# Kernel tuning notes

Measured on AMD Instinct MI355X. Metric: run time of the kernel, lower is better.

Reference implementation:

```python
import jax, jax.numpy as jnp
import numpy as np

B, S, H, M, E = 8, 2048, 2048, 256, 8
Hh = H // 2

def setup_inputs() -> dict:
    key = jax.random.key(0)
    ks = jax.random.split(key, 12)
    s = 0.02
    return {
        "x":   jax.random.normal(ks[0], (B, S, H), dtype=jnp.float32),
        # metacognitive (router) network: H -> M -> M -> E, softmax
        "Wm1": jax.random.normal(ks[1], (H, M), dtype=jnp.float32) * s,
        "bm1": jnp.zeros((M,), dtype=jnp.float32),
        "Wm2": jax.random.normal(ks[2], (M, M), dtype=jnp.float32) * s,
        "bm2": jnp.zeros((M,), dtype=jnp.float32),
        "Wm3": jax.random.normal(ks[3], (M, E), dtype=jnp.float32) * s,
        "bm3": jnp.zeros((E,), dtype=jnp.float32),
        # stacked expert MLPs: Linear(H,H/2)-ReLU-Linear(H/2,H)-Tanh
        "W1":  jax.random.normal(ks[4], (E, H, Hh), dtype=jnp.float32) * s,
        "b1":  jnp.zeros((E, Hh), dtype=jnp.float32),
        "W2":  jax.random.normal(ks[5], (E, Hh, H), dtype=jnp.float32) * s,
        "b2":  jnp.zeros((E, H), dtype=jnp.float32),
        # strategy_effectiveness buffer (init: ones)
        "eff": jnp.ones((E,), dtype=jnp.float32),
    }

def reference(x, Wm1, bm1, Wm2, bm2, Wm3, bm3, W1, b1, W2, b2, eff):
    # --- select_strategy ---
    pooled = x.mean(axis=1)                                   # [B,H]
    h = jax.nn.relu(pooled @ Wm1 + bm1)                       # [B,M]
    h = jax.nn.relu(h @ Wm2 + bm2)                            # [B,M]
    probs = jax.nn.softmax(h @ Wm3 + bm3, axis=-1)            # [B,E]
    w = jax.nn.softmax(probs * eff[None, :], axis=-1)         # [B,E]
    # --- apply_strategies (all experts batched) ---
    he = jax.nn.relu(jnp.einsum('bsh,ehf->bsef', x, W1) + b1) # [B,S,E,Hh]
    ye = jnp.tanh(jnp.einsum('bsef,efh->bseh', he, W2) + b2)  # [B,S,E,H]
    out = jnp.einsum('bseh,be->bsh', ye, w)                   # [B,S,H]
    return out
```

## Files before the change

### kernel.cpp

```cpp
#include <hip/hip_runtime.h>
#include <hip/hip_bf16.h>
#include <cstdint>
#include <cstddef>

#define B_   8
#define S_   2048
#define H_   2048
#define M_   256
#define E_   8
#define HH_  1024
#define BS_  (B_*S_)

typedef _Float16 f16;
typedef _Float16 f16x8 __attribute__((ext_vector_type(8)));
typedef float    f32x4 __attribute__((ext_vector_type(4)));

#define SLOT_B   49152
#define A_HALF_B 16384
#define B_OFF    32768
#define B_HALF_B 8192

__device__ __forceinline__ void gl_lds16(const void* g, void* l) {
  __builtin_amdgcn_global_load_lds(
      (const __attribute__((address_space(1))) uint32_t*)g,
      (__attribute__((address_space(3))) uint32_t*)l, 16, 0, 0);
}

__device__ __forceinline__ int sinv(int P) {
  int b8 = (P >> 8) & 1, b7 = (P >> 7) & 1, b6 = (P >> 6) & 1;
  return P ^ (b8 << 6) ^ (b7 << 5) ^ ((b6 ^ b8) << 4);
}

__device__ __forceinline__ float fast_tanh(float x) {
  x = fminf(fmaxf(x, -15.f), 15.f);
  float t = __expf(2.f * x);
  return (t - 1.f) / (t + 1.f);
}

template<int NG, int NT_LG, int ASEG_SH, int BSEG_SH, class F>
__device__ __forceinline__ void kloop(const char* aS0, const char* aS1,
    const char* bS0, char* ldsc, int aRd, int bRd, int wv, int ln,
    f32x4 (&acc)[4][4], F fold) {
  constexpr int NT = 1 << NT_LG;

  auto stage = [&](int gs, int ss, int h) {
    int tt = gs & (NT - 1);
    size_t ea = 0, eb = 0;
    if constexpr (ASEG_SH != 0) {
      int e = gs >> NT_LG;
      ea = (size_t)e << ASEG_SH;
      eb = (size_t)e << BSEG_SH;
    }
    int koff = tt * 128 + h * 64;
    char* dA = ldsc + ss * SLOT_B + h * A_HALF_B + wv * 1024 + ln * 16;
    gl_lds16(aS0 + ea + koff, dA);
    gl_lds16(aS1 + ea + koff, dA + 8192);
    char* dB = ldsc + ss * SLOT_B + B_OFF + h * B_HALF_B + wv * 1024 + ln * 16;
    gl_lds16(bS0 + eb + koff, dB);
  };

#pragma unroll
  for (int t = 0; t < 2; ++t) { stage(t, t, 0); stage(t, t, 1); }
  asm volatile("s_waitcnt vmcnt(6)" ::: "memory");
  __builtin_amdgcn_s_barrier();

  int s = 0;
#pragma unroll 1
  for (int g = 0; g < NG; ++g) {
    int ss = s + 2; if (ss >= 3) ss -= 3;
    const char* sbase = ldsc + s * SLOT_B;
    __builtin_amdgcn_sched_barrier(0);

    f16x8 af[2][4], bf[2][4];
#pragma unroll
    for (int h = 0; h < 2; ++h) {
      const char* aB = sbase + h * A_HALF_B + aRd;
      const char* bB = sbase + B_OFF + h * B_HALF_B + bRd;
#pragma unroll
      for (int m = 0; m < 4; ++m) af[h][m] = *(const f16x8*)(aB + m * 1024);
#pragma unroll
      for (int n = 0; n < 4; ++n) bf[h][n] = *(const f16x8*)(bB + n * 1024);
    }

    if ((g + 2) < NG) { stage(g + 2, ss, 0); stage(g + 2, ss, 1); }

    __builtin_amdgcn_s_setprio(1);
#pragma unroll
    for (int h = 0; h < 2; ++h)
#pragma unroll
      for (int m = 0; m < 4; ++m)
#pragma unroll
        for (int n = 0; n < 4; ++n)
          acc[m][n] = __builtin_amdgcn_mfma_f32_16x16x32_f16(af[h][m], bf[h][n], acc[m][n], 0, 0, 0);
    __builtin_amdgcn_s_setprio(0);

    if ((g & (NT - 1)) == (NT - 1)) fold(g >> NT_LG);

    __builtin_amdgcn_sched_barrier(0);
    if (g < NG - 2) { asm volatile("s_waitcnt vmcnt(6)" ::: "memory"); }
    else            { asm volatile("s_waitcnt vmcnt(0)" ::: "memory"); }
    __builtin_amdgcn_s_barrier();
    ++s; if (s >= 3) s -= 3;
  }
}

__global__ __launch_bounds__(512, 2) void gemm1_pipe(
    const f16* __restrict__ xf, const f16* __restrict__ W1t,
    const float* __restrict__ b1, f16* __restrict__ he) {
  __shared__ f16 lds[3 * 24576];
  char* ldsc = (char*)lds;
  int tid = threadIdx.x, wv = tid >> 6, ln = tid & 63, l15 = ln & 15, kq = ln >> 4;
  int wr = wv >> 1, wc = wv & 1;

  int id = blockIdx.x;
  int logical = (id & 7) * 512 + (id >> 3);
  int nt = logical & 7, mt = (logical >> 3) & 63, e = logical >> 9;
  int brow = mt * 256, bcol = nt * 128;

  int mask = (ln & 7) << 4;
  int aRd = ((wr * 64 + l15) * 64 + kq * 16) ^ mask;
  int bRd = ((wc * 64 + l15) * 64 + kq * 16) ^ mask;

  int PA0 = wv * 1024 + ln * 16;
  int LA0 = sinv(PA0), LA1 = sinv(PA0 + 8192), LB = sinv(PA0);
  const char* aS0 = (const char*)xf + (size_t)(brow + (LA0 >> 6)) * (H_ * 2) + (LA0 & 63);
  const char* aS1 = (const char*)xf + (size_t)(brow + (LA1 >> 6)) * (H_ * 2) + (LA1 & 63);
  const char* bS0 = (const char*)W1t + ((size_t)e * HH_ + bcol + (LB >> 6)) * (H_ * 2) + (LB & 63);

  f32x4 acc[4][4] = {};
  kloop<32, 5, 0, 0>(aS0, aS1, bS0, ldsc, aRd, bRd, wv, ln, acc, [](int) {});

  f16* C = he + (size_t)e * BS_ * HH_;
#pragma unroll
  for (int n = 0; n < 4; ++n) {
    int gc = bcol + wc * 64 + n * 16 + l15;
    float bias = b1[e * HH_ + gc];
#pragma unroll
    for (int m = 0; m < 4; ++m) {
      int gr0 = brow + wr * 64 + m * 16 + kq * 4;
#pragma unroll
      for (int r = 0; r < 4; ++r)
        C[(size_t)(gr0 + r) * HH_ + gc] = (f16)fmaxf(acc[m][n][r] + bias, 0.f);
    }
  }
}

__global__ __launch_bounds__(512, 2) void gemm2_pipe(
    const f16* __restrict__ he, const f16* __restrict__ W2t,
    const float* __restrict__ b2, const float* __restrict__ wbuf,
    float* __restrict__ out) {
  __shared__ f16 lds[3 * 24576];
  __shared__ float biasLDS[E_][128];
  __shared__ float wLDS[E_];
  char* ldsc = (char*)lds;
  int tid = threadIdx.x, wv = tid >> 6, ln = tid & 63, l15 = ln & 15, kq = ln >> 4;
  int wr = wv >> 1, wc = wv & 1;

  int id = blockIdx.x;
  int logical = (id & 7) * 128 + (id >> 3);
  int nt = logical & 15, mt = logical >> 4;
  int brow = mt * 256, bcol = nt * 128;
  int bb = brow >> 11;

  {
    int i = tid;
#pragma unroll
    for (int rep = 0; rep < 2; ++rep, i += 512) {
      int e = i >> 7, c = i & 127;
      biasLDS[e][c] = b2[e * H_ + bcol + c];
    }
    if (tid < E_) wLDS[tid] = wbuf[bb * E_ + tid];
  }
  __syncthreads();

  int mask = (ln & 7) << 4;
  int aRd = ((wr * 64 + l15) * 64 + kq * 16) ^ mask;
  int bRd = ((wc * 64 + l15) * 64 + kq * 16) ^ mask;

  int PA0 = wv * 1024 + ln * 16;
  int LA0 = sinv(PA0), LA1 = sinv(PA0 + 8192), LB = sinv(PA0);
  const char* aS0 = (const char*)he + (size_t)(brow + (LA0 >> 6)) * (HH_ * 2) + (LA0 & 63);
  const char* aS1 = (const char*)he + (size_t)(brow + (LA1 >> 6)) * (HH_ * 2) + (LA1 & 63);
  const char* bS0 = (const char*)W2t + (size_t)(bcol + (LB >> 6)) * (HH_ * 2) + (LB & 63);

  f32x4 acc[4][4] = {};
  f32x4 tot[4][4] = {};

  auto fold = [&](int e) {
    float we = wLDS[e];
#pragma unroll
    for (int n = 0; n < 4; ++n) {
      float bias = biasLDS[e][wc * 64 + n * 16 + l15];
#pragma unroll
      for (int m = 0; m < 4; ++m) {
#pragma unroll
        for (int r = 0; r < 4; ++r) {
          tot[m][n][r] += we * fast_tanh(acc[m][n][r] + bias);
          acc[m][n][r] = 0.f;
        }
      }
    }
  };

  kloop<128, 4, 25, 22>(aS0, aS1, bS0, ldsc, aRd, bRd, wv, ln, acc, fold);

#pragma unroll
  for (int n = 0; n < 4; ++n) {
    int gc = bcol + wc * 64 + n * 16 + l15;
#pragma unroll
    for (int m = 0; m < 4; ++m) {
      int gr0 = brow + wr * 64 + m * 16 + kq * 4;
#pragma unroll
      for (int r = 0; r < 4; ++r)
        out[(size_t)(gr0 + r) * H_ + gc] = tot[m][n][r];
    }
  }
}

__global__ void convert_x_pool(const float* __restrict__ x, f16* __restrict__ xf,
                               float* __restrict__ partial) {
  int h  = blockIdx.x * 256 + threadIdx.x;
  int sc = blockIdx.y;
  int b  = blockIdx.z;
  size_t base = ((size_t)b * S_ + sc * 64) * H_ + h;
  float sum = 0.f;
#pragma unroll 4
  for (int i = 0; i < 64; ++i) {
    float v = x[base + (size_t)i * H_];
    sum += v;
    xf[base + (size_t)i * H_] = (f16)v;
  }
  partial[((size_t)b * H_ + h) * 32 + sc] = sum;
}

__global__ void pool_finalize(const float* __restrict__ partial, float* __restrict__ pooled) {
  int i = blockIdx.x * 256 + threadIdx.x;
  float s = 0.f;
#pragma unroll
  for (int c = 0; c < 32; ++c) s += partial[(size_t)i * 32 + c];
  pooled[i] = s * (1.0f / S_);
}

__global__ void router_kernel(const float* __restrict__ pooled,
                              const float* __restrict__ Wm1, const float* __restrict__ bm1,
                              const float* __restrict__ Wm2, const float* __restrict__ bm2,
                              const float* __restrict__ Wm3, const float* __restrict__ bm3,
                              const float* __restrict__ eff, float* __restrict__ wout) {
  __shared__ float pl[H_];
  __shared__ float h1[M_];
  __shared__ float h2[M_];
  __shared__ float lg[E_];
  int b = blockIdx.x;
  int t = threadIdx.x;

  for (int i = t; i < H_; i += 256) pl[i] = pooled[b * H_ + i];
  __syncthreads();

  float s = bm1[t];
  for (int k = 0; k < H_; ++k) s += pl[k] * Wm1[(size_t)k * M_ + t];
  h1[t] = fmaxf(s, 0.f);
  __syncthreads();

  s = bm2[t];
  for (int k = 0; k < M_; ++k) s += h1[k] * Wm2[k * M_ + t];
  h2[t] = fmaxf(s, 0.f);
  __syncthreads();

  if (t < E_) {
    float l = bm3[t];
    for (int k = 0; k < M_; ++k) l += h2[k] * Wm3[k * E_ + t];
    lg[t] = l;
  }
  __syncthreads();

  if (t == 0) {
    float p[E_], q[E_];
    float mx = -1e30f;
    for (int e = 0; e < E_; ++e) mx = fmaxf(mx, lg[e]);
    float den = 0.f;
    for (int e = 0; e < E_; ++e) { p[e] = __expf(lg[e] - mx); den += p[e]; }
    float inv = 1.f / den;
    for (int e = 0; e < E_; ++e) q[e] = p[e] * inv * eff[e];
    mx = -1e30f;
    for (int e = 0; e < E_; ++e) mx = fmaxf(mx, q[e]);
    den = 0.f;
    for (int e = 0; e < E_; ++e) { q[e] = __expf(q[e] - mx); den += q[e]; }
    inv = 1.f / den;
    for (int e = 0; e < E_; ++e) wout[b * E_ + e] = q[e] * inv;
  }
}

__global__ void transpose_cvt(const float* __restrict__ in, f16* __restrict__ out,
                              int R, int C) {
  __shared__ f16 tile[32][33];
  int e  = blockIdx.z;
  int c0 = blockIdx.x * 32, r0 = blockIdx.y * 32;
  int tx = threadIdx.x & 31, ty = threadIdx.x >> 5;
  const float* inp = in + (size_t)e * R * C;
  f16* outp = out + (size_t)e * R * C;
#pragma unroll
  for (int i = 0; i < 4; ++i) {
    int r = r0 + ty + i * 8;
    tile[ty + i * 8][tx] = (f16)inp[(size_t)r * C + c0 + tx];
  }
  __syncthreads();
#pragma unroll
  for (int i = 0; i < 4; ++i) {
    int c = c0 + ty + i * 8;
    outp[(size_t)c * R + r0 + tx] = tile[tx][ty + i * 8];
  }
}

extern "C" void kernel_launch(void* const* d_in, const int* in_sizes, int n_in,
                              void* d_out, int out_size, void* d_ws, size_t ws_size,
                              hipStream_t stream) {
  const float* x   = (const float*)d_in[0];
  const float* Wm1 = (const float*)d_in[1];
  const float* bm1 = (const float*)d_in[2];
  const float* Wm2 = (const float*)d_in[3];
  const float* bm2 = (const float*)d_in[4];
  const float* Wm3 = (const float*)d_in[5];
  const float* bm3 = (const float*)d_in[6];
  const float* W1  = (const float*)d_in[7];
  const float* b1  = (const float*)d_in[8];
  const float* W2  = (const float*)d_in[9];
  const float* b2  = (const float*)d_in[10];
  const float* eff = (const float*)d_in[11];
  float* out = (float*)d_out;

  char* ws = (char*)d_ws;
  size_t off = 0;
  auto take = [&](size_t bytes) { void* p = ws + off; off += (bytes + 255) & ~(size_t)255; return p; };

  f16*   xf      = (f16*)  take((size_t)BS_ * H_ * 2);
  f16*   W1t     = (f16*)  take((size_t)E_ * HH_ * H_ * 2);
  f16*   W2t     = (f16*)  take((size_t)E_ * H_ * HH_ * 2);
  float* partial = (float*)take((size_t)B_ * H_ * 32 * 4);
  float* pooled  = (float*)take((size_t)B_ * H_ * 4);
  float* wbuf    = (float*)take(1024);
  f16*   he      = (f16*)  take((size_t)E_ * BS_ * HH_ * 2);

  convert_x_pool<<<dim3(H_ / 256, S_ / 64, B_), 256, 0, stream>>>(x, xf, partial);
  pool_finalize<<<(B_ * H_) / 256, 256, 0, stream>>>(partial, pooled);
  router_kernel<<<B_, 256, 0, stream>>>(pooled, Wm1, bm1, Wm2, bm2, Wm3, bm3, eff, wbuf);
  transpose_cvt<<<dim3(HH_ / 32, H_ / 32, E_), 256, 0, stream>>>(W1, W1t, H_, HH_);
  transpose_cvt<<<dim3(H_ / 32, HH_ / 32, E_), 256, 0, stream>>>(W2, W2t, HH_, H_);

  gemm1_pipe<<<4096, 512, 0, stream>>>(xf, W1t, b1, he);
  gemm2_pipe<<<1024, 512, 0, stream>>>(he, W2t, b2, wbuf, out);
}
```

Measured before the change: 1.483 ms.

## Enlarge GEMM tiles to 256x256 with 4-slot half-K pipeline

Both expert GEMMs move from 256x128 to 256x256 block tiles, so each wave computes 128x64 (8x4 MFMA tiles) and operands are reused more per LDS load. The K-loop is restructured into 32-element half-steps across a 4-slot LDS ring with 3-ahead prefetch, a simpler XOR swizzle, and staging interleaved per M-half with extra barriers. The gemm2 running weighted-tanh accumulator is stored in fp16 to save registers, which lowers output precision. The larger accumulator footprint raises register pressure at two blocks per CU.

```diff
diff --git a/kernel.cpp b/kernel.cpp
--- a/kernel.cpp
+++ b/kernel.cpp
@@ -13,12 +13,10 @@
 
 typedef _Float16 f16;
 typedef _Float16 f16x8 __attribute__((ext_vector_type(8)));
+typedef _Float16 f16x4 __attribute__((ext_vector_type(4)));
 typedef float    f32x4 __attribute__((ext_vector_type(4)));
 
-#define SLOT_B   49152
-#define A_HALF_B 16384
-#define B_OFF    32768
-#define B_HALF_B 8192
+#define HSLOT 32768
 
 __device__ __forceinline__ void gl_lds16(const void* g, void* l) {
   __builtin_amdgcn_global_load_lds(
@@ -26,118 +24,126 @@
       (__attribute__((address_space(3))) uint32_t*)l, 16, 0, 0);
 }
 
-__device__ __forceinline__ int sinv(int P) {
-  int b8 = (P >> 8) & 1, b7 = (P >> 7) & 1, b6 = (P >> 6) & 1;
-  return P ^ (b8 << 6) ^ (b7 << 5) ^ ((b6 ^ b8) << 4);
-}
-
 __device__ __forceinline__ float fast_tanh(float x) {
   x = fminf(fmaxf(x, -15.f), 15.f);
   float t = __expf(2.f * x);
   return (t - 1.f) / (t + 1.f);
 }
 
-template<int NG, int NT_LG, int ASEG_SH, int BSEG_SH, class F>
-__device__ __forceinline__ void kloop(const char* aS0, const char* aS1,
-    const char* bS0, char* ldsc, int aRd, int bRd, int wv, int ln,
-    f32x4 (&acc)[4][4], F fold) {
-  constexpr int NT = 1 << NT_LG;
-
-  auto stage = [&](int gs, int ss, int h) {
-    int tt = gs & (NT - 1);
-    size_t ea = 0, eb = 0;
-    if constexpr (ASEG_SH != 0) {
-      int e = gs >> NT_LG;
-      ea = (size_t)e << ASEG_SH;
-      eb = (size_t)e << BSEG_SH;
-    }
-    int koff = tt * 128 + h * 64;
-    char* dA = ldsc + ss * SLOT_B + h * A_HALF_B + wv * 1024 + ln * 16;
-    gl_lds16(aS0 + ea + koff, dA);
-    gl_lds16(aS1 + ea + koff, dA + 8192);
-    char* dB = ldsc + ss * SLOT_B + B_OFF + h * B_HALF_B + wv * 1024 + ln * 16;
-    gl_lds16(bS0 + eb + koff, dB);
+template<int NG, bool SEG, int KB, class F>
+__device__ __forceinline__ void kloop(const char* aBlk, const char* bBlk,
+                                      char* ldsc, f32x4 (&acc)[8][4], F&& fold) {
+  constexpr int NH = NG * 2;
+  const int tid = threadIdx.x, ln = tid & 63, wv = tid >> 6;
+  const int l15 = ln & 15, kq = ln >> 4;
+  const int wm = wv >> 2, wn = wv & 3;
+
+  const char* aPc[2]; const char* bPc[2];
+#pragma unroll
+  for (int j = 0; j < 2; ++j) {
+    int row = (tid >> 2) + j * 128;
+    int kqs = (tid & 3) ^ ((row >> 1) & 3);
+    aPc[j] = aBlk + (size_t)row * KB + kqs * 16;
+    bPc[j] = bBlk + (size_t)row * KB + kqs * 16;
+  }
+  const int rowA = wm * 128 + l15;
+  const int rowB = wn * 64 + l15;
+  const int aRd = rowA * 64 + ((kq ^ ((rowA >> 1) & 3)) << 4);
+  const int bRd = 16384 + rowB * 64 + ((kq ^ ((rowB >> 1) & 3)) << 4);
+  const int dst0 = tid * 16;
+
+  auto stage2 = [&](int Ht, int op) {
+    if (Ht >= NH) return;
+    char* sb = ldsc + (Ht & 3) * HSLOT;
+    size_t oa, ob;
+    if constexpr (SEG) {
+      size_t kb = (size_t)((Ht & 31) * 64);
+      oa = ((size_t)(Ht >> 5) << 25) + kb;
+      ob = ((size_t)(Ht >> 5) << 22) + kb;
+    } else { oa = ob = (size_t)Ht * 64; }
+    if (op == 0) {
+      gl_lds16(aPc[0] + oa, sb + dst0);
+      gl_lds16(aPc[1] + oa, sb + 8192 + dst0);
+    } else {
+      gl_lds16(bPc[0] + ob, sb + 16384 + dst0);
+      gl_lds16(bPc[1] + ob, sb + 24576 + dst0);
+    }
   };
 
 #pragma unroll
-  for (int t = 0; t < 2; ++t) { stage(t, t, 0); stage(t, t, 1); }
-  asm volatile("s_waitcnt vmcnt(6)" ::: "memory");
+  for (int Ht = 0; Ht < 3; ++Ht) { stage2(Ht, 0); stage2(Ht, 1); }
+  asm volatile("s_waitcnt vmcnt(8)" ::: "memory");
   __builtin_amdgcn_s_barrier();
 
-  int s = 0;
 #pragma unroll 1
   for (int g = 0; g < NG; ++g) {
-    int ss = s + 2; if (ss >= 3) ss -= 3;
-    const char* sbase = ldsc + s * SLOT_B;
-    __builtin_amdgcn_sched_barrier(0);
-
-    f16x8 af[2][4], bf[2][4];
-#pragma unroll
-    for (int h = 0; h < 2; ++h) {
-      const char* aB = sbase + h * A_HALF_B + aRd;
-      const char* bB = sbase + B_OFF + h * B_HALF_B + bRd;
-#pragma unroll
-      for (int m = 0; m < 4; ++m) af[h][m] = *(const f16x8*)(aB + m * 1024);
-#pragma unroll
-      for (int n = 0; n < 4; ++n) bf[h][n] = *(const f16x8*)(bB + n * 1024);
-    }
-
-    if ((g + 2) < NG) { stage(g + 2, ss, 0); stage(g + 2, ss, 1); }
-
-    __builtin_amdgcn_s_setprio(1);
-#pragma unroll
-    for (int h = 0; h < 2; ++h)
-#pragma unroll
-      for (int m = 0; m < 4; ++m)
-#pragma unroll
-        for (int n = 0; n < 4; ++n)
-          acc[m][n] = __builtin_amdgcn_mfma_f32_16x16x32_f16(af[h][m], bf[h][n], acc[m][n], 0, 0, 0);
-    __builtin_amdgcn_s_setprio(0);
-
-    if ((g & (NT - 1)) == (NT - 1)) fold(g >> NT_LG);
-
-    __builtin_amdgcn_sched_barrier(0);
-    if (g < NG - 2) { asm volatile("s_waitcnt vmcnt(6)" ::: "memory"); }
-    else            { asm volatile("s_waitcnt vmcnt(0)" ::: "memory"); }
-    __builtin_amdgcn_s_barrier();
-    ++s; if (s >= 3) s -= 3;
-  }
-}
-
-__global__ __launch_bounds__(512, 2) void gemm1_pipe(
+#pragma unroll
+    for (int kh = 0; kh < 2; ++kh) {
+      const int H = g * 2 + kh;
+      const char* sb = ldsc + (H & 3) * HSLOT;
+      f16x8 bf[4];
+#pragma unroll
+      for (int mh = 0; mh < 2; ++mh) {
+        f16x8 af[4];
+        const char* ab = sb + aRd + mh * 4096;
+#pragma unroll
+        for (int m = 0; m < 4; ++m) af[m] = *(const f16x8*)(ab + m * 1024);
+        if (mh == 0) {
+          const char* bb = sb + bRd;
+#pragma unroll
+          for (int n = 0; n < 4; ++n) bf[n] = *(const f16x8*)(bb + n * 1024);
+        }
+        stage2(H + 3, mh);
+        __builtin_amdgcn_s_barrier();
+        asm volatile("s_waitcnt lgkmcnt(0)" ::: "memory");
+        __builtin_amdgcn_sched_barrier(0);
+        __builtin_amdgcn_s_setprio(1);
+#pragma unroll
+        for (int m = 0; m < 4; ++m)
+#pragma unroll
+          for (int n = 0; n < 4; ++n)
+            acc[mh * 4 + m][n] = __builtin_amdgcn_mfma_f32_16x16x32_f16(
+                af[m], bf[n], acc[mh * 4 + m][n], 0, 0, 0);
+        __builtin_amdgcn_s_setprio(0);
+        __builtin_amdgcn_sched_barrier(0);
+        if (mh == 1) {
+          if (H < NH - 3)       { asm volatile("s_waitcnt vmcnt(8)" ::: "memory"); }
+          else if (H == NH - 3) { asm volatile("s_waitcnt vmcnt(4)" ::: "memory"); }
+          else if (H == NH - 2) { asm volatile("s_waitcnt vmcnt(0)" ::: "memory"); }
+        }
+        __builtin_amdgcn_s_barrier();
+      }
+    }
+    if constexpr (SEG) { if ((g & 15) == 15) fold(g >> 4); }
+  }
+}
+
+__global__ __launch_bounds__(512, 2) void gemm1_t8(
     const f16* __restrict__ xf, const f16* __restrict__ W1t,
     const float* __restrict__ b1, f16* __restrict__ he) {
-  __shared__ f16 lds[3 * 24576];
-  char* ldsc = (char*)lds;
-  int tid = threadIdx.x, wv = tid >> 6, ln = tid & 63, l15 = ln & 15, kq = ln >> 4;
-  int wr = wv >> 1, wc = wv & 1;
-
+  __shared__ alignas(16) char ldsc[4 * HSLOT];
   int id = blockIdx.x;
-  int logical = (id & 7) * 512 + (id >> 3);
-  int nt = logical & 7, mt = (logical >> 3) & 63, e = logical >> 9;
-  int brow = mt * 256, bcol = nt * 128;
-
-  int mask = (ln & 7) << 4;
-  int aRd = ((wr * 64 + l15) * 64 + kq * 16) ^ mask;
-  int bRd = ((wc * 64 + l15) * 64 + kq * 16) ^ mask;
-
-  int PA0 = wv * 1024 + ln * 16;
-  int LA0 = sinv(PA0), LA1 = sinv(PA0 + 8192), LB = sinv(PA0);
-  const char* aS0 = (const char*)xf + (size_t)(brow + (LA0 >> 6)) * (H_ * 2) + (LA0 & 63);
-  const char* aS1 = (const char*)xf + (size_t)(brow + (LA1 >> 6)) * (H_ * 2) + (LA1 & 63);
-  const char* bS0 = (const char*)W1t + ((size_t)e * HH_ + bcol + (LB >> 6)) * (H_ * 2) + (LB & 63);
-
-  f32x4 acc[4][4] = {};
-  kloop<32, 5, 0, 0>(aS0, aS1, bS0, ldsc, aRd, bRd, wv, ln, acc, [](int) {});
-
-  f16* C = he + (size_t)e * BS_ * HH_;
+  int logical = (id & 7) * 256 + (id >> 3);
+  int e = logical >> 8, mt = (logical >> 2) & 63, nt = logical & 3;
+  int brow = mt * 256, bcol = nt * 256;
+
+  const char* aBlk = (const char*)xf + (size_t)brow * 4096;
+  const char* bBlk = (const char*)W1t + ((size_t)e << 22) + (size_t)bcol * 4096;
+
+  f32x4 acc[8][4] = {};
+  kloop<32, false, 4096>(aBlk, bBlk, ldsc, acc, [](int) {});
+
+  const int tid = threadIdx.x, ln = tid & 63, wv = tid >> 6;
+  const int l15 = ln & 15, kq4 = (ln >> 4) * 4;
+  const int wm = wv >> 2, wn = wv & 3;
+  f16* C = he + ((size_t)e << 24);
 #pragma unroll
   for (int n = 0; n < 4; ++n) {
-    int gc = bcol + wc * 64 + n * 16 + l15;
+    int gc = bcol + wn * 64 + n * 16 + l15;
     float bias = b1[e * HH_ + gc];
 #pragma unroll
-    for (int m = 0; m < 4; ++m) {
-      int gr0 = brow + wr * 64 + m * 16 + kq * 4;
+    for (int m = 0; m < 8; ++m) {
+      int gr0 = brow + wm * 128 + m * 16 + kq4;
 #pragma unroll
       for (int r = 0; r < 4; ++r)
         C[(size_t)(gr0 + r) * HH_ + gc] = (f16)fmaxf(acc[m][n][r] + bias, 0.f);
@@ -145,74 +151,65 @@
   }
 }
 
-__global__ __launch_bounds__(512, 2) void gemm2_pipe(
+__global__ __launch_bounds__(512, 2) void gemm2_t8(
     const f16* __restrict__ he, const f16* __restrict__ W2t,
     const float* __restrict__ b2, const float* __restrict__ wbuf,
     float* __restrict__ out) {
-  __shared__ f16 lds[3 * 24576];
-  __shared__ float biasLDS[E_][128];
+  __shared__ alignas(16) char ldsc[4 * HSLOT];
+  __shared__ float biasLDS[E_][256];
   __shared__ float wLDS[E_];
-  char* ldsc = (char*)lds;
-  int tid = threadIdx.x, wv = tid >> 6, ln = tid & 63, l15 = ln & 15, kq = ln >> 4;
-  int wr = wv >> 1, wc = wv & 1;
-
   int id = blockIdx.x;
-  int logical = (id & 7) * 128 + (id >> 3);
-  int nt = logical & 15, mt = logical >> 4;
-  int brow = mt * 256, bcol = nt * 128;
+  int logical = (id & 7) * 64 + (id >> 3);
+  int mt = logical >> 3, nt = logical & 7;
+  int brow = mt * 256, bcol = nt * 256;
   int bb = brow >> 11;
+
+  const int tid = threadIdx.x, ln = tid & 63, wv = tid >> 6;
+  const int l15 = ln & 15, kq4 = (ln >> 4) * 4;
+  const int wm = wv >> 2, wn = wv & 3;
 
   {
     int i = tid;
 #pragma unroll
-    for (int rep = 0; rep < 2; ++rep, i += 512) {
-      int e = i >> 7, c = i & 127;
-      biasLDS[e][c] = b2[e * H_ + bcol + c];
-    }
+    for (int rep = 0; rep < 4; ++rep, i += 512)
+      biasLDS[i >> 8][i & 255] = b2[(size_t)(i >> 8) * H_ + bcol + (i & 255)];
     if (tid < E_) wLDS[tid] = wbuf[bb * E_ + tid];
   }
   __syncthreads();
 
-  int mask = (ln & 7) << 4;
-  int aRd = ((wr * 64 + l15) * 64 + kq * 16) ^ mask;
-  int bRd = ((wc * 64 + l15) * 64 + kq * 16) ^ mask;
-
-  int PA0 = wv * 1024 + ln * 16;
-  int LA0 = sinv(PA0), LA1 = sinv(PA0 + 8192), LB = sinv(PA0);
-  const char* aS0 = (const char*)he + (size_t)(brow + (LA0 >> 6)) * (HH_ * 2) + (LA0 & 63);
-  const char* aS1 = (const char*)he + (size_t)(brow + (LA1 >> 6)) * (HH_ * 2) + (LA1 & 63);
-  const char* bS0 = (const char*)W2t + (size_t)(bcol + (LB >> 6)) * (HH_ * 2) + (LB & 63);
-
-  f32x4 acc[4][4] = {};
-  f32x4 tot[4][4] = {};
+  const char* aBlk = (const char*)he + (size_t)brow * 2048;
+  const char* bBlk = (const char*)W2t + (size_t)bcol * 2048;
+
+  f32x4 acc[8][4] = {};
+  f16x4 tot[8][4] = {};
 
   auto fold = [&](int e) {
     float we = wLDS[e];
 #pragma unroll
     for (int n = 0; n < 4; ++n) {
-      float bias = biasLDS[e][wc * 64 + n * 16 + l15];
-#pragma unroll
-      for (int m = 0; m < 4; ++m) {
+      float bias = biasLDS[e][wn * 64 + n * 16 + l15];
+#pragma unroll
+      for (int m = 0; m < 8; ++m) {
 #pragma unroll
         for (int r = 0; r < 4; ++r) {
-          tot[m][n][r] += we * fast_tanh(acc[m][n][r] + bias);
+          tot[m][n][r] += (f16)(we * fast_tanh(acc[m][n][r] + bias));
           acc[m][n][r] = 0.f;
         }
       }
     }
   };
 
-  kloop<128, 4, 25, 22>(aS0, aS1, bS0, ldsc, aRd, bRd, wv, ln, acc, fold);
+  kloop<128, true, 2048>(aBlk, bBlk, ldsc, acc, fold);
 
 #pragma unroll
   for (int n = 0; n < 4; ++n) {
-    int gc = bcol + wc * 64 + n * 16 + l15;
-#pragma unroll
-    for (int m = 0; m < 4; ++m) {
-      int gr0 = brow + wr * 64 + m * 16 + kq * 4;
+    int gc = bcol + wn * 64 + n * 16 + l15;
+#pragma unroll
+    for (int m = 0; m < 8; ++m) {
+      int gr0 = brow + wm * 128 + m * 16 + kq4;
 #pragma unroll
       for (int r = 0; r < 4; ++r)
-        out[(size_t)(gr0 + r) * H_ + gc] = tot[m][n][r];
+        out[(size_t)(gr0 + r) * H_ + gc] = (float)tot[m][n][r];
     }
   }
 }
@@ -346,6 +343,6 @@
   transpose_cvt<<<dim3(HH_ / 32, H_ / 32, E_), 256, 0, stream>>>(W1, W1t, H_, HH_);
   transpose_cvt<<<dim3(H_ / 32, HH_ / 32, E_), 256, 0, stream>>>(W2, W2t, HH_, H_);
 
-  gemm1_pipe<<<4096, 512, 0, stream>>>(xf, W1t, b1, he);
-  gemm2_pipe<<<1024, 512, 0, stream>>>(he, W2t, b2, wbuf, out);
-}
+  gemm1_t8<<<2048, 512, 0, stream>>>(xf, W1t, b1, he);
+  gemm2_t8<<<512, 512, 0, stream>>>(he, W2t, b2, wbuf, out);
+}
```

New measurement: 1.412 ms. 1.05x faster.
